# Performance work log

Hardware: AMD Instinct MI355X
Metric: run time of the kernel (lower is better)

## Reference

```python
import jax, jax.numpy as jnp
import numpy as np

B, S, D, H, V = 32, 1024, 512, 4, 8185
DH = 3 * D // H  # 384 per-head projection; q/k/v each 128
FFN = 4 * D
LN_EPS = 1e-3  # keras LayerNormalization default epsilon


def _pos_encoding(seq_len, d_model):
    pos = np.arange(seq_len)[:, None].astype(np.float32)
    i = np.arange(d_model)[None, :].astype(np.float32)
    angles = pos / np.power(10000.0, 2.0 * (i // 2) / np.float32(d_model))
    angles[:, 0::2] = np.sin(angles[:, 0::2])
    angles[:, 1::2] = np.cos(angles[:, 1::2])
    return jnp.asarray(angles, dtype=jnp.float32)  # [S, D]


def _layernorm(x, g, b):
    mu = jnp.mean(x, axis=-1, keepdims=True)
    var = jnp.mean(jnp.square(x - mu), axis=-1, keepdims=True)
    return (x - mu) * jax.lax.rsqrt(var + LN_EPS) * g + b


def setup_inputs() -> dict:
    key = jax.random.key(0)
    ks = jax.random.split(key, 8)
    sc = 0.02
    return {
        "inputs": jax.random.randint(ks[0], (B, S), 0, V, dtype=jnp.int32),
        "emb": jax.random.normal(ks[1], (V, D), jnp.float32) * sc,
        "Wp": jax.random.normal(ks[2], (H, D, DH), jnp.float32) * sc,
        "bp": jnp.zeros((H, DH), jnp.float32),
        "Wo": jax.random.normal(ks[3], (D, D), jnp.float32) * sc,
        "bo": jnp.zeros((D,), jnp.float32),
        "ln1_g": jnp.ones((D,), jnp.float32),
        "ln1_b": jnp.zeros((D,), jnp.float32),
        "W1": jax.random.normal(ks[4], (D, FFN), jnp.float32) * sc,
        "b1": jnp.zeros((FFN,), jnp.float32),
        "W2": jax.random.normal(ks[5], (FFN, D), jnp.float32) * sc,
        "b2": jnp.zeros((D,), jnp.float32),
        "ln2_g": jnp.ones((D,), jnp.float32),
        "ln2_b": jnp.zeros((D,), jnp.float32),
        "Wh": jax.random.normal(ks[6], (D, D), jnp.float32) * sc,
        "bh": jnp.zeros((D,), jnp.float32),
        "Wf": jax.random.normal(ks[7], (D, 1), jnp.float32) * sc,
        "bf": jnp.zeros((1,), jnp.float32),
    }


def reference(inputs, emb, Wp, bp, Wo, bo, ln1_g, ln1_b, W1, b1, W2, b2,
              ln2_g, ln2_b, Wh, bh, Wf, bf):
    b, s = inputs.shape
    x = emb[inputs] + _pos_encoding(s, emb.shape[1])[None]  # [B,S,D]

    # decoder block: batched per-head projections (q|k|v packed along last axis)
    res = x
    d = jnp.einsum('bsd,hde->bhse', x, Wp) + bp[:, None, :]  # [B,H,S,3*dh]
    q, k, v = jnp.split(d, 3, axis=-1)  # each [B,H,S,dh]
    # NOTE: source scales by rsqrt(seq_len) (tf.shape(k)[1]), not head dim
    scale = jax.lax.rsqrt(jnp.float32(s))
    scores = jnp.einsum('bhse,bhte->bhst', q, k) * scale  # [B,H,S,S]
    heads = jnp.einsum('bhst,bhte->bhse', scores, v)  # linear attn (no softmax)
    concat = heads.transpose(0, 2, 1, 3).reshape(b, s, -1)  # [B,S,D]
    attn = concat @ Wo + bo
    x = _layernorm(attn + res, ln1_g, ln1_b)
    h = jax.nn.relu(x @ W1 + b1) @ W2 + b2
    x = _layernorm(h + x, ln2_g, ln2_b)

    # classification head on first token
    x0 = x[:, 0]
    hid = jax.nn.relu(x0 @ Wh + bh)
    logits = hid @ Wf + bf  # [B,1]
    return logits, jax.nn.sigmoid(logits)
```

## Files before the change

kernel.cpp:

```cpp
#include <hip/hip_runtime.h>
#include <hip/hip_bf16.h>

__global__ __launch_bounds__(256) void qr_k(
    const int* __restrict__ inp, const float* __restrict__ emb,
    const float* __restrict__ Wp, const float* __restrict__ bp,
    float* __restrict__ X0, float* __restrict__ r, float* __restrict__ alpha,
    float* __restrict__ Acc, int* __restrict__ Cnt)
{
    __shared__ float xs[512];
    __shared__ float red[256];
    __shared__ float q0s[128];
    int b = blockIdx.x, h = blockIdx.y, t = threadIdx.x;
    if (b == 0 && h == 0) {
        if (t < 32) Acc[t] = 0.f;
        else if (t < 64) Cnt[t - 32] = 0;
    }
    int tok0 = inp[b * 1024];
#pragma unroll
    for (int rep = 0; rep < 2; rep++) {
        int d = t + rep * 256;
        float v = emb[(long)tok0 * 512 + d] + ((d & 1) ? 1.0f : 0.0f);
        xs[d] = v;
        if (h == 0) X0[b * 512 + d] = v;
    }
    __syncthreads();

    int f = t & 127, dh = t >> 7;
    const float* wq = Wp + (long)h * 196608 + f;
    float acc = 0.f;
#pragma unroll 8
    for (int d = dh * 256; d < dh * 256 + 256; d++)
        acc += xs[d] * wq[(long)d * 384];
    red[t] = acc;
    __syncthreads();
    if (t < 128) q0s[t] = red[t] + red[t + 128] + bp[h * 384 + t];
    __syncthreads();
    if (t < 128) red[t] = q0s[t] * bp[h * 384 + 128 + t];
    __syncthreads();
    for (int w = 64; w >= 1; w >>= 1) {
        if (t < w) red[t] += red[t + w];
        __syncthreads();
    }
    if (t == 0) alpha[b * 4 + h] = red[0];

    const float4* q4 = (const float4*)q0s;
#pragma unroll
    for (int rep = 0; rep < 2; rep++) {
        int d = t + rep * 256;
        const float4* wr = (const float4*)(Wp + ((long)(h * 512 + d)) * 384 + 128);
        float a2 = 0.f;
#pragma unroll 8
        for (int f4 = 0; f4 < 32; f4++) {
            float4 w = wr[f4], qq = q4[f4];
            a2 += w.x * qq.x + w.y * qq.y + w.z * qq.z + w.w * qq.w;
        }
        r[((long)(b * 4 + h)) * 512 + d] = a2;
    }
}

__global__ __launch_bounds__(256) void xu_k(
    const int* __restrict__ inp, const float* __restrict__ emb,
    const float* __restrict__ r, const float* __restrict__ alpha,
    float* __restrict__ Tpp, float* __restrict__ Gp)
{
    __shared__ float xs[32 * 516];
    __shared__ float rs[4 * 520];
    __shared__ float us[128];
    __shared__ int  toks[32];
    int b = blockIdx.x, sg = blockIdx.y, t = threadIdx.x;
    int wave = t >> 6, lane = t & 63;

#pragma unroll
    for (int i = 0; i < 2; i++) {
        int idx = t + i * 256;
        int h = idx >> 7, k4 = idx & 127;
        *(float4*)&rs[h * 520 + k4 * 4] =
            *(const float4*)&r[((long)(b * 4 + h)) * 512 + k4 * 4];
    }

    float w4[4];
#pragma unroll
    for (int j = 0; j < 4; j++) {
        float expo = (float)(lane * 8 + j * 2) * (1.0f / 512.0f);
        w4[j] = exp2f(-expo * 13.287712379549449f);
    }

    float accT[4][2] = {};
    float gacc = 0.f;
    for (int it = 0; it < 2; it++) {
        int s0 = (sg * 2 + it) * 32;
        __syncthreads();
        if (t < 32) toks[t] = inp[b * 1024 + s0 + t];
        __syncthreads();

#pragma unroll
        for (int i = 0; i < 8; i++) {
            int row = wave * 8 + i;
            float s = (float)(s0 + row);
            int tok = toks[row];
            const float4* e = (const float4*)&emb[(long)tok * 512 + lane * 8];
            float4 e0 = e[0], e1 = e[1];
            float sv[4], cv[4];
#pragma unroll
            for (int j = 0; j < 4; j++) {
                float ang = s * w4[j];
                sv[j] = __sinf(ang);
                cv[j] = __cosf(ang);
            }
            *(float4*)&xs[row * 516 + lane * 8] =
                make_float4(e0.x + sv[0], e0.y + cv[0], e0.z + sv[1], e0.w + cv[1]);
            *(float4*)&xs[row * 516 + lane * 8 + 4] =
                make_float4(e1.x + sv[2], e1.y + cv[2], e1.z + sv[3], e1.w + cv[3]);
        }
        __syncthreads();

        {
            int s = t >> 3, h = (t >> 1) & 3, half = t & 1;
            const float* xrow = xs + s * 516 + half * 256;
            const float* rrow = rs + h * 520 + half * 256;
            float acc = 0.f;
#pragma unroll 8
            for (int k = 0; k < 64; k++) {
                float4 xv = *(const float4*)&xrow[k * 4];
                float4 rv = *(const float4*)&rrow[k * 4];
                acc += xv.x * rv.x + xv.y * rv.y + xv.z * rv.z + xv.w * rv.w;
            }
            acc += __shfl_xor(acc, 1);
            if (half == 0) us[s * 4 + h] = acc + alpha[b * 4 + h];
        }
        __syncthreads();

        if (t < 4) {
#pragma unroll
            for (int s = 0; s < 32; s++) gacc += us[s * 4 + t];
        }

#pragma unroll 4
        for (int s = 0; s < 32; s++) {
            float x0 = xs[s * 516 + t];
            float x1 = xs[s * 516 + 256 + t];
#pragma unroll
            for (int h = 0; h < 4; h++) {
                float uv = us[s * 4 + h];
                accT[h][0] += uv * x0;
                accT[h][1] += uv * x1;
            }
        }
    }
    long base = (long)(b * 16 + sg) * 2048;
#pragma unroll
    for (int h = 0; h < 4; h++) {
        Tpp[base + h * 512 + t] = accT[h][0];
        Tpp[base + h * 512 + 256 + t] = accT[h][1];
    }
    if (t < 4) Gp[(b * 16 + sg) * 4 + t] = gacc;
}

__global__ __launch_bounds__(256) void att1_k(
    const float* __restrict__ Tpp, const float* __restrict__ Gp,
    const float* __restrict__ Wp, const float* __restrict__ bp,
    float* __restrict__ C0)
{
    __shared__ float tps[512];
    __shared__ float red[256];
    int b = blockIdx.x, jt = blockIdx.y, t = threadIdx.x;
    int h = jt >> 1, e0 = (jt & 1) * 64;
#pragma unroll
    for (int i = 0; i < 2; i++) {
        int d = t + i * 256;
        float v = 0.f;
#pragma unroll 8
        for (int sg = 0; sg < 16; sg++)
            v += Tpp[(long)b * 32768 + sg * 2048 + h * 512 + d];
        tps[d] = v;
    }
    __syncthreads();
    int e = e0 + (t & 63), rg = t >> 6;
    const float* wv = Wp + (long)h * 196608 + 256 + e;
    float acc = 0.f;
#pragma unroll 8
    for (int d = rg * 128; d < rg * 128 + 128; d++)
        acc += tps[d] * wv[(long)d * 384];
    red[t] = acc;
    __syncthreads();
    if (t < 64) {
        float gam = 0.f;
#pragma unroll
        for (int sg = 0; sg < 16; sg++) gam += Gp[(b * 16 + sg) * 4 + h];
        float sum = red[t] + red[t + 64] + red[t + 128] + red[t + 192];
        float c = 0.03125f * (sum + gam * bp[h * 384 + 256 + e0 + t]);
        C0[b * 512 + h * 128 + e0 + t] = c;
    }
}

__global__ __launch_bounds__(256) void att2s_k(
    const float* __restrict__ C0, const float* __restrict__ Wo,
    const float* __restrict__ bo, const float* __restrict__ X0,
    float* __restrict__ A1, float* __restrict__ Stat)
{
    __shared__ float c0s[512];
    __shared__ float red[256];
    int b = blockIdx.x, jt = blockIdx.y, t = threadIdx.x;
    c0s[t] = C0[b * 512 + t];
    c0s[t + 256] = C0[b * 512 + t + 256];
    __syncthreads();
    int j = jt * 64 + (t & 63), rg = t >> 6;
    float acc = 0.f;
#pragma unroll 8
    for (int d = rg * 128; d < rg * 128 + 128; d++)
        acc += c0s[d] * Wo[(long)d * 512 + j];
    red[t] = acc;
    __syncthreads();
    if (t < 64) {
        int jj = jt * 64 + t;
        float a = red[t] + red[t + 64] + red[t + 128] + red[t + 192]
                + bo[jj] + X0[b * 512 + jj];
        A1[b * 512 + jj] = a;
        float s = a, q = a * a;
#pragma unroll
        for (int off = 32; off; off >>= 1) {
            s += __shfl_down(s, off);
            q += __shfl_down(q, off);
        }
        if (t == 0) {
            Stat[(b * 8 + jt) * 2]     = s;
            Stat[(b * 8 + jt) * 2 + 1] = q;
        }
    }
}

__global__ __launch_bounds__(256) void ffn1_k(
    const float* __restrict__ A1, const float* __restrict__ Stat,
    const float* __restrict__ g1, const float* __restrict__ b1v,
    const float* __restrict__ W1, float* __restrict__ Hp1)
{
    __shared__ float at[32][128];
    __shared__ float mrs[32][2];
    int jt = blockIdx.x, ks = blockIdx.y, t = threadIdx.x;
    if (t < 32) {
        float s = 0.f, q = 0.f;
#pragma unroll
        for (int p8 = 0; p8 < 8; p8++) {
            s += Stat[(t * 8 + p8) * 2];
            q += Stat[(t * 8 + p8) * 2 + 1];
        }
        float mean = s * (1.0f / 512.0f);
        float var = q * (1.0f / 512.0f) - mean * mean;
        mrs[t][0] = mean;
        mrs[t][1] = rsqrtf(var + 0.001f);
    }
    __syncthreads();
#pragma unroll
    for (int i = 0; i < 4; i++) {
        int idx = t + i * 256;
        int row = idx >> 5, f4 = idx & 31;
        int col = ks * 128 + f4 * 4;
        float4 a4 = *(const float4*)&A1[(long)row * 512 + col];
        float4 g4 = *(const float4*)&g1[col];
        float4 bb = *(const float4*)&b1v[col];
        float mean = mrs[row][0], rstd = mrs[row][1];
        float4 v;
        v.x = (a4.x - mean) * rstd * g4.x + bb.x;
        v.y = (a4.y - mean) * rstd * g4.y + bb.y;
        v.z = (a4.z - mean) * rstd * g4.z + bb.z;
        v.w = (a4.w - mean) * rstd * g4.w + bb.w;
        ((float4*)at)[idx] = v;
    }
    __syncthreads();
    int j = jt * 64 + (t & 63), rg = t >> 6;
    float acc[8] = {};
    const float* wp = W1 + (long)(ks * 128) * 2048 + j;
#pragma unroll 4
    for (int k = 0; k < 128; k++) {
        float wv = wp[(long)k * 2048];
#pragma unroll
        for (int rr = 0; rr < 8; rr++)
            acc[rr] += at[rg * 8 + rr][k] * wv;
    }
#pragma unroll
    for (int rr = 0; rr < 8; rr++)
        Hp1[((long)(ks * 32 + rg * 8 + rr)) * 2048 + j] = acc[rr];
}

__global__ __launch_bounds__(256) void ffn2_k(
    const float* __restrict__ Hp1, const float* __restrict__ b1,
    const float* __restrict__ W2, float* __restrict__ Hp2)
{
    __shared__ float at[32][128];
    int jt = blockIdx.x, ks = blockIdx.y, t = threadIdx.x;
#pragma unroll
    for (int i = 0; i < 4; i++) {
        int idx = t + i * 256;
        int row = idx >> 5, f4 = idx & 31;
        int col4 = ks * 32 + f4;
        float4 v = ((const float4*)b1)[col4];
#pragma unroll
        for (int p = 0; p < 4; p++) {
            float4 pv = ((const float4*)Hp1)[(long)p * 16384 + (long)row * 512 + col4];
            v.x += pv.x; v.y += pv.y; v.z += pv.z; v.w += pv.w;
        }
        v.x = fmaxf(v.x, 0.f); v.y = fmaxf(v.y, 0.f);
        v.z = fmaxf(v.z, 0.f); v.w = fmaxf(v.w, 0.f);
        ((float4*)at)[idx] = v;
    }
    __syncthreads();
    int j = jt * 64 + (t & 63), rg = t >> 6;
    float acc[8] = {};
    const float* wp = W2 + (long)(ks * 128) * 512 + j;
#pragma unroll 4
    for (int k = 0; k < 128; k++) {
        float wv = wp[(long)k * 512];
#pragma unroll
        for (int rr = 0; rr < 8; rr++)
            acc[rr] += at[rg * 8 + rr][k] * wv;
    }
#pragma unroll
    for (int rr = 0; rr < 8; rr++)
        Hp2[((long)(ks * 32 + rg * 8 + rr)) * 512 + j] = acc[rr];
}

__global__ __launch_bounds__(256) void headp3_k(
    const float* __restrict__ Hp2, const float* __restrict__ b2,
    const float* __restrict__ A1, const float* __restrict__ Stat,
    const float* __restrict__ g1v, const float* __restrict__ b1v,
    const float* __restrict__ g2v, const float* __restrict__ b2v,
    const float* __restrict__ Wh, const float* __restrict__ bh,
    const float* __restrict__ Wf, const float* __restrict__ bf,
    float* __restrict__ Acc, int* __restrict__ Cnt, float* __restrict__ out)
{
    __shared__ float xs[512];
    __shared__ float red[256];
    __shared__ float sd[8];
    __shared__ float mr[2];
    int b = blockIdx.x, jt = blockIdx.y, t = threadIdx.x;
    if (t == 0) {
        float s = 0.f, q = 0.f;
#pragma unroll
        for (int p8 = 0; p8 < 8; p8++) {
            s += Stat[(b * 8 + p8) * 2];
            q += Stat[(b * 8 + p8) * 2 + 1];
        }
        float mean = s * (1.0f / 512.0f);
        mr[0] = mean;
        mr[1] = rsqrtf(q * (1.0f / 512.0f) - mean * mean + 0.001f);
    }
    __syncthreads();
    float mean1 = mr[0], rstd1 = mr[1];
    float a[2];
#pragma unroll
    for (int rep = 0; rep < 2; rep++) {
        int j = t + rep * 256;
        float y1 = (A1[b * 512 + j] - mean1) * rstd1 * g1v[j] + b1v[j];
        float v = b2[j] + y1;
#pragma unroll
        for (int ks = 0; ks < 16; ks++)
            v += Hp2[((long)(ks * 32 + b)) * 512 + j];
        a[rep] = v;
    }
    float s = a[0] + a[1];
#pragma unroll
    for (int off = 32; off; off >>= 1) s += __shfl_down(s, off);
    if ((t & 63) == 0) sd[t >> 6] = s;
    __syncthreads();
    float mean = (sd[0] + sd[1] + sd[2] + sd[3]) * (1.0f / 512.0f);
    float d0 = a[0] - mean, d1 = a[1] - mean;
    float v2 = d0 * d0 + d1 * d1;
#pragma unroll
    for (int off = 32; off; off >>= 1) v2 += __shfl_down(v2, off);
    if ((t & 63) == 0) sd[4 + (t >> 6)] = v2;
    __syncthreads();
    float var = (sd[4] + sd[5] + sd[6] + sd[7]) * (1.0f / 512.0f);
    float rstd = rsqrtf(var + 0.001f);
    xs[t] = d0 * rstd * g2v[t] + b2v[t];
    xs[t + 256] = d1 * rstd * g2v[t + 256] + b2v[t + 256];
    __syncthreads();

    int j = jt * 64 + (t & 63), rg = t >> 6;
    const float* w = Wh + j;
    float acc = 0.f;
#pragma unroll 8
    for (int d = rg * 128; d < rg * 128 + 128; d++)
        acc += xs[d] * w[(long)d * 512];
    red[t] = acc;
    __syncthreads();
    if (t < 64) {
        int jj = jt * 64 + t;
        float hid = red[t] + red[t + 64] + red[t + 128] + red[t + 192] + bh[jj];
        hid = fmaxf(hid, 0.f);
        float p = hid * Wf[jj];
#pragma unroll
        for (int off = 32; off; off >>= 1) p += __shfl_down(p, off);
        if (t == 0) {
            atomicAdd(&Acc[b], p);
            __threadfence();
            int old = atomicAdd(&Cnt[b], 1);
            if (old == 7) {
                float tot = atomicAdd(&Acc[b], 0.0f);
                float logit = tot + bf[0];
                out[b] = logit;
                out[32 + b] = 1.f / (1.f + expf(-logit));
            }
        }
    }
}

extern "C" void kernel_launch(void* const* d_in, const int* in_sizes, int n_in,
                              void* d_out, int out_size, void* d_ws, size_t ws_size,
                              hipStream_t stream)
{
    const int*   inputs = (const int*)  d_in[0];
    const float* emb    = (const float*)d_in[1];
    const float* Wp     = (const float*)d_in[2];
    const float* bp     = (const float*)d_in[3];
    const float* Wo     = (const float*)d_in[4];
    const float* bo     = (const float*)d_in[5];
    const float* ln1_g  = (const float*)d_in[6];
    const float* ln1_b  = (const float*)d_in[7];
    const float* W1     = (const float*)d_in[8];
    const float* b1     = (const float*)d_in[9];
    const float* W2     = (const float*)d_in[10];
    const float* b2     = (const float*)d_in[11];
    const float* ln2_g  = (const float*)d_in[12];
    const float* ln2_b  = (const float*)d_in[13];
    const float* Wh     = (const float*)d_in[14];
    const float* bh     = (const float*)d_in[15];
    const float* Wf     = (const float*)d_in[16];
    const float* bf     = (const float*)d_in[17];
    float* out = (float*)d_out;

    char* p = (char*)d_ws;
    float* X0    = (float*)p;  p += 65536;
    float* r     = (float*)p;  p += 262144;
    float* alpha = (float*)p;  p += 1024;
    float* Gp    = (float*)p;  p += 8192;
    float* Tpp   = (float*)p;  p += 4194304;
    float* C0    = (float*)p;  p += 65536;
    float* A1    = (float*)p;  p += 65536;
    float* Stat  = (float*)p;  p += 2048;
    float* Acc   = (float*)p;  p += 512;
    int*   Cnt   = (int*)p;    p += 512;
    float* Hp1   = (float*)p;  p += 1048576;
    float* Hp2   = (float*)p;  p += 1048576;

    qr_k<<<dim3(32, 4), 256, 0, stream>>>(inputs, emb, Wp, bp, X0, r, alpha,
                                          Acc, Cnt);
    xu_k<<<dim3(32, 16), 256, 0, stream>>>(inputs, emb, r, alpha, Tpp, Gp);
    att1_k<<<dim3(32, 8), 256, 0, stream>>>(Tpp, Gp, Wp, bp, C0);
    att2s_k<<<dim3(32, 8), 256, 0, stream>>>(C0, Wo, bo, X0, A1, Stat);
    ffn1_k<<<dim3(32, 4), 256, 0, stream>>>(A1, Stat, ln1_g, ln1_b, W1, Hp1);
    ffn2_k<<<dim3(8, 16), 256, 0, stream>>>(Hp1, b1, W2, Hp2);
    headp3_k<<<dim3(32, 8), 256, 0, stream>>>(Hp2, b2, A1, Stat,
                                              ln1_g, ln1_b, ln2_g, ln2_b,
                                              Wh, bh, Wf, bf, Acc, Cnt, out);
}
```

Measured before the change: 199.2 us.

## Register-resident xu_k attention accumulation and finer split-K for FFN kernels

```diff
diff --git a/kernel.cpp b/kernel.cpp
--- a/kernel.cpp
+++ b/kernel.cpp
@@ -63,21 +63,21 @@
     const float* __restrict__ r, const float* __restrict__ alpha,
     float* __restrict__ Tpp, float* __restrict__ Gp)
 {
-    __shared__ float xs[32 * 516];
-    __shared__ float rs[4 * 520];
-    __shared__ float us[128];
-    __shared__ int  toks[32];
+    __shared__ float redT[4][4][64][8];
+    __shared__ float redG[4][4];
     int b = blockIdx.x, sg = blockIdx.y, t = threadIdx.x;
     int wave = t >> 6, lane = t & 63;
 
-#pragma unroll
-    for (int i = 0; i < 2; i++) {
-        int idx = t + i * 256;
-        int h = idx >> 7, k4 = idx & 127;
-        *(float4*)&rs[h * 520 + k4 * 4] =
-            *(const float4*)&r[((long)(b * 4 + h)) * 512 + k4 * 4];
-    }
-
+    float rsv[4][8];
+    float al[4];
+#pragma unroll
+    for (int h = 0; h < 4; h++) {
+        const float4* rp = (const float4*)&r[((long)(b * 4 + h)) * 512 + lane * 8];
+        float4 r0 = rp[0], r1 = rp[1];
+        rsv[h][0] = r0.x; rsv[h][1] = r0.y; rsv[h][2] = r0.z; rsv[h][3] = r0.w;
+        rsv[h][4] = r1.x; rsv[h][5] = r1.y; rsv[h][6] = r1.z; rsv[h][7] = r1.w;
+        al[h] = alpha[b * 4 + h];
+    }
     float w4[4];
 #pragma unroll
     for (int j = 0; j < 4; j++) {
@@ -85,75 +85,81 @@
         w4[j] = exp2f(-expo * 13.287712379549449f);
     }
 
-    float accT[4][2] = {};
-    float gacc = 0.f;
-    for (int it = 0; it < 2; it++) {
-        int s0 = (sg * 2 + it) * 32;
-        __syncthreads();
-        if (t < 32) toks[t] = inp[b * 1024 + s0 + t];
-        __syncthreads();
-
-#pragma unroll
-        for (int i = 0; i < 8; i++) {
-            int row = wave * 8 + i;
-            float s = (float)(s0 + row);
-            int tok = toks[row];
+    float accT[4][8] = {};
+    float gacc[4] = {};
+    int s0 = sg * 64 + wave * 16;
+#pragma unroll
+    for (int g = 0; g < 4; g++) {
+        float xv[4][8];
+        float up[4][4];
+#pragma unroll
+        for (int i = 0; i < 4; i++) {
+            int srow = s0 + g * 4 + i;
+            int tok = inp[b * 1024 + srow];
             const float4* e = (const float4*)&emb[(long)tok * 512 + lane * 8];
             float4 e0 = e[0], e1 = e[1];
+            float sf = (float)srow;
             float sv[4], cv[4];
 #pragma unroll
             for (int j = 0; j < 4; j++) {
-                float ang = s * w4[j];
+                float ang = sf * w4[j];
                 sv[j] = __sinf(ang);
                 cv[j] = __cosf(ang);
             }
-            *(float4*)&xs[row * 516 + lane * 8] =
-                make_float4(e0.x + sv[0], e0.y + cv[0], e0.z + sv[1], e0.w + cv[1]);
-            *(float4*)&xs[row * 516 + lane * 8 + 4] =
-                make_float4(e1.x + sv[2], e1.y + cv[2], e1.z + sv[3], e1.w + cv[3]);
-        }
-        __syncthreads();
-
-        {
-            int s = t >> 3, h = (t >> 1) & 3, half = t & 1;
-            const float* xrow = xs + s * 516 + half * 256;
-            const float* rrow = rs + h * 520 + half * 256;
-            float acc = 0.f;
-#pragma unroll 8
-            for (int k = 0; k < 64; k++) {
-                float4 xv = *(const float4*)&xrow[k * 4];
-                float4 rv = *(const float4*)&rrow[k * 4];
-                acc += xv.x * rv.x + xv.y * rv.y + xv.z * rv.z + xv.w * rv.w;
+            xv[i][0] = e0.x + sv[0]; xv[i][1] = e0.y + cv[0];
+            xv[i][2] = e0.z + sv[1]; xv[i][3] = e0.w + cv[1];
+            xv[i][4] = e1.x + sv[2]; xv[i][5] = e1.y + cv[2];
+            xv[i][6] = e1.z + sv[3]; xv[i][7] = e1.w + cv[3];
+#pragma unroll
+            for (int h = 0; h < 4; h++) {
+                float acc = 0.f;
+#pragma unroll
+                for (int jj = 0; jj < 8; jj++) acc += xv[i][jj] * rsv[h][jj];
+                up[i][h] = acc;
             }
-            acc += __shfl_xor(acc, 1);
-            if (half == 0) us[s * 4 + h] = acc + alpha[b * 4 + h];
-        }
-        __syncthreads();
-
-        if (t < 4) {
-#pragma unroll
-            for (int s = 0; s < 32; s++) gacc += us[s * 4 + t];
-        }
-
-#pragma unroll 4
-        for (int s = 0; s < 32; s++) {
-            float x0 = xs[s * 516 + t];
-            float x1 = xs[s * 516 + 256 + t];
+        }
+#pragma unroll
+        for (int off = 32; off; off >>= 1) {
+#pragma unroll
+            for (int i = 0; i < 4; i++)
+#pragma unroll
+                for (int h = 0; h < 4; h++)
+                    up[i][h] += __shfl_xor(up[i][h], off);
+        }
+#pragma unroll
+        for (int i = 0; i < 4; i++) {
 #pragma unroll
             for (int h = 0; h < 4; h++) {
-                float uv = us[s * 4 + h];
-                accT[h][0] += uv * x0;
-                accT[h][1] += uv * x1;
+                float u = up[i][h] + al[h];
+                gacc[h] += u;
+#pragma unroll
+                for (int jj = 0; jj < 8; jj++) accT[h][jj] += u * xv[i][jj];
             }
         }
     }
+#pragma unroll
+    for (int h = 0; h < 4; h++) {
+        *(float4*)&redT[wave][h][lane][0] =
+            make_float4(accT[h][0], accT[h][1], accT[h][2], accT[h][3]);
+        *(float4*)&redT[wave][h][lane][4] =
+            make_float4(accT[h][4], accT[h][5], accT[h][6], accT[h][7]);
+    }
+    if (lane == 0) {
+#pragma unroll
+        for (int h = 0; h < 4; h++) redG[wave][h] = gacc[h];
+    }
+    __syncthreads();
     long base = (long)(b * 16 + sg) * 2048;
 #pragma unroll
-    for (int h = 0; h < 4; h++) {
-        Tpp[base + h * 512 + t] = accT[h][0];
-        Tpp[base + h * 512 + 256 + t] = accT[h][1];
-    }
-    if (t < 4) Gp[(b * 16 + sg) * 4 + t] = gacc;
+    for (int k = 0; k < 8; k++) {
+        int idx = t + k * 256;
+        int h = idx >> 9, d = idx & 511;
+        float v = redT[0][h][d >> 3][d & 7] + redT[1][h][d >> 3][d & 7]
+                + redT[2][h][d >> 3][d & 7] + redT[3][h][d >> 3][d & 7];
+        Tpp[base + idx] = v;
+    }
+    if (t < 4) Gp[(b * 16 + sg) * 4 + t] =
+        redG[0][t] + redG[1][t] + redG[2][t] + redG[3][t];
 }
 
 __global__ __launch_bounds__(256) void att1_k(
@@ -234,7 +240,7 @@
     const float* __restrict__ g1, const float* __restrict__ b1v,
     const float* __restrict__ W1, float* __restrict__ Hp1)
 {
-    __shared__ float at[32][128];
+    __shared__ float at[32][32];
     __shared__ float mrs[32][2];
     int jt = blockIdx.x, ks = blockIdx.y, t = threadIdx.x;
     if (t < 32) {
@@ -250,11 +256,9 @@
         mrs[t][1] = rsqrtf(var + 0.001f);
     }
     __syncthreads();
-#pragma unroll
-    for (int i = 0; i < 4; i++) {
-        int idx = t + i * 256;
-        int row = idx >> 5, f4 = idx & 31;
-        int col = ks * 128 + f4 * 4;
+    {
+        int row = t >> 3, f4 = t & 7;
+        int col = ks * 32 + f4 * 4;
         float4 a4 = *(const float4*)&A1[(long)row * 512 + col];
         float4 g4 = *(const float4*)&g1[col];
         float4 bb = *(const float4*)&b1v[col];
@@ -264,14 +268,14 @@
         v.y = (a4.y - mean) * rstd * g4.y + bb.y;
         v.z = (a4.z - mean) * rstd * g4.z + bb.z;
         v.w = (a4.w - mean) * rstd * g4.w + bb.w;
-        ((float4*)at)[idx] = v;
+        ((float4*)at)[t] = v;
     }
     __syncthreads();
     int j = jt * 64 + (t & 63), rg = t >> 6;
     float acc[8] = {};
-    const float* wp = W1 + (long)(ks * 128) * 2048 + j;
-#pragma unroll 4
-    for (int k = 0; k < 128; k++) {
+    const float* wp = W1 + (long)(ks * 32) * 2048 + j;
+#pragma unroll 8
+    for (int k = 0; k < 32; k++) {
         float wv = wp[(long)k * 2048];
 #pragma unroll
         for (int rr = 0; rr < 8; rr++)
@@ -286,29 +290,27 @@
     const float* __restrict__ Hp1, const float* __restrict__ b1,
     const float* __restrict__ W2, float* __restrict__ Hp2)
 {
-    __shared__ float at[32][128];
-    int jt = blockIdx.x, ks = blockIdx.y, t = threadIdx.x;
-#pragma unroll
-    for (int i = 0; i < 4; i++) {
-        int idx = t + i * 256;
-        int row = idx >> 5, f4 = idx & 31;
-        int col4 = ks * 32 + f4;
+    __shared__ float at[32][32];
+    int jt = blockIdx.x, ks2 = blockIdx.y, t = threadIdx.x;
+    {
+        int row = t >> 3, f4 = t & 7;
+        int col4 = ks2 * 8 + f4;
         float4 v = ((const float4*)b1)[col4];
 #pragma unroll
-        for (int p = 0; p < 4; p++) {
-            float4 pv = ((const float4*)Hp1)[(long)p * 16384 + (long)row * 512 + col4];
+        for (int p = 0; p < 16; p++) {
+            float4 pv = ((const float4*)Hp1)[(long)p * 16384 + row * 512 + col4];
             v.x += pv.x; v.y += pv.y; v.z += pv.z; v.w += pv.w;
         }
         v.x = fmaxf(v.x, 0.f); v.y = fmaxf(v.y, 0.f);
         v.z = fmaxf(v.z, 0.f); v.w = fmaxf(v.w, 0.f);
-        ((float4*)at)[idx] = v;
+        ((float4*)at)[t] = v;
     }
     __syncthreads();
     int j = jt * 64 + (t & 63), rg = t >> 6;
     float acc[8] = {};
-    const float* wp = W2 + (long)(ks * 128) * 512 + j;
-#pragma unroll 4
-    for (int k = 0; k < 128; k++) {
+    const float* wp = W2 + (long)(ks2 * 32) * 512 + j;
+#pragma unroll 8
+    for (int k = 0; k < 32; k++) {
         float wv = wp[(long)k * 512];
 #pragma unroll
         for (int rr = 0; rr < 8; rr++)
@@ -316,7 +318,7 @@
     }
 #pragma unroll
     for (int rr = 0; rr < 8; rr++)
-        Hp2[((long)(ks * 32 + rg * 8 + rr)) * 512 + j] = acc[rr];
+        Hp2[((long)(ks2 * 32 + rg * 8 + rr)) * 512 + j] = acc[rr];
 }
 
 __global__ __launch_bounds__(256) void headp3_k(
@@ -352,8 +354,8 @@
         int j = t + rep * 256;
         float y1 = (A1[b * 512 + j] - mean1) * rstd1 * g1v[j] + b1v[j];
         float v = b2[j] + y1;
-#pragma unroll
-        for (int ks = 0; ks < 16; ks++)
+#pragma unroll 16
+        for (int ks = 0; ks < 64; ks++)
             v += Hp2[((long)(ks * 32 + b)) * 512 + j];
         a[rep] = v;
     }
@@ -439,16 +441,16 @@
     float* Stat  = (float*)p;  p += 2048;
     float* Acc   = (float*)p;  p += 512;
     int*   Cnt   = (int*)p;    p += 512;
-    float* Hp1   = (float*)p;  p += 1048576;
-    float* Hp2   = (float*)p;  p += 1048576;
+    float* Hp1   = (float*)p;  p += 4194304;
+    float* Hp2   = (float*)p;  p += 4194304;
 
     qr_k<<<dim3(32, 4), 256, 0, stream>>>(inputs, emb, Wp, bp, X0, r, alpha,
                                           Acc, Cnt);
     xu_k<<<dim3(32, 16), 256, 0, stream>>>(inputs, emb, r, alpha, Tpp, Gp);
     att1_k<<<dim3(32, 8), 256, 0, stream>>>(Tpp, Gp, Wp, bp, C0);
     att2s_k<<<dim3(32, 8), 256, 0, stream>>>(C0, Wo, bo, X0, A1, Stat);
-    ffn1_k<<<dim3(32, 4), 256, 0, stream>>>(A1, Stat, ln1_g, ln1_b, W1, Hp1);
-    ffn2_k<<<dim3(8, 16), 256, 0, stream>>>(Hp1, b1, W2, Hp2);
+    ffn1_k<<<dim3(32, 16), 256, 0, stream>>>(A1, Stat, ln1_g, ln1_b, W1, Hp1);
+    ffn2_k<<<dim3(8, 64), 256, 0, stream>>>(Hp1, b1, W2, Hp2);
     headp3_k<<<dim3(32, 8), 256, 0, stream>>>(Hp2, b2, A1, Stat,
                                               ln1_g, ln1_b, ln2_g, ln2_b,
                                               Wh, bh, Wf, bf, Acc, Cnt, out);
```

New measurement: 187.0 us. 1.07x faster.
